# Kernel tuning notes

Hardware: AMD Instinct MI355X
Metric: run time of the kernel (lower is better)

Reference implementation:

```python
import jax, jax.numpy as jnp
import numpy as np

D_MODEL = 1024
N_HEADS = 16
D_KEYS = 64
GROUP_POSITIONS = [list(range(g * 32, (g + 1) * 32)) for g in range(4)]


def _make_tables(group_positions, dim):
    # InGroup table: pe[j,i] = (j/Lg) * L0 / 10000^(2*(i//2)/dim)
    L0 = len(group_positions[0])
    rows = []
    for grp in group_positions:
        Lg = len(grp)
        for j in range(Lg):
            rows.append([j / Lg * L0 / np.power(10000.0, 2 * (i // 2) / dim) for i in range(dim)])
    pe = np.array(rows)
    ingroup = np.concatenate([np.sin(pe[:, 0::2]), np.cos(pe[:, 1::2])], axis=1).astype(np.float32)
    # Sequence (group) table: pe[j,i] = grp[0] / 10000^(j/Lg), constant over i
    rows = []
    for grp in group_positions:
        Lg = len(grp)
        for j in range(Lg):
            rows.append([grp[0] / np.power(10000.0, j / Lg) for _ in range(dim)])
    pe = np.array(rows)
    seq = np.concatenate([np.sin(pe[:, 0::2]), np.cos(pe[:, 1::2])], axis=1).astype(np.float32)
    return jnp.asarray(ingroup), jnp.asarray(seq)


def setup_inputs() -> dict:
    key = jax.random.key(0)
    ks = jax.random.split(key, 12)
    B, L, S = 64, 128, 128
    dqk = D_KEYS * N_HEADS
    sc_in = 1.0 / np.sqrt(D_MODEL)
    sc_out = 1.0 / np.sqrt(dqk)
    inp = {
        "queries": jax.random.normal(ks[0], (B, L, D_MODEL), jnp.float32),
        "keys": jax.random.normal(ks[1], (B, S, D_MODEL), jnp.float32),
        "values": jax.random.normal(ks[2], (B, S, D_MODEL), jnp.float32),
        "attn_mask": jnp.zeros((B, 1, L, S), dtype=bool),
        "Wq": jax.random.normal(ks[3], (D_MODEL, dqk), jnp.float32) * sc_in,
        "bq": jnp.zeros((dqk,), jnp.float32),
        "Wk": jax.random.normal(ks[4], (D_MODEL, dqk), jnp.float32) * sc_in,
        "bk": jnp.zeros((dqk,), jnp.float32),
        "Wv": jax.random.normal(ks[5], (D_MODEL, dqk), jnp.float32) * sc_in,
        "bv": jnp.zeros((dqk,), jnp.float32),
        "Wo": jax.random.normal(ks[6], (dqk, D_MODEL), jnp.float32) * sc_out,
        "bo": jnp.zeros((D_MODEL,), jnp.float32),
    }
    pos_ingroup, pos_seq = _make_tables(GROUP_POSITIONS, D_KEYS)
    inp["pos_ingroup"] = pos_ingroup  # [n_pos, d_keys]
    inp["pos_seq"] = pos_seq          # [n_pos, d_keys]
    return inp


def _rope(x, pos):
    # x: [B, H, L, D]; pos: [L, D]
    sin, cos = jnp.split(pos, 2, axis=-1)
    sin_pos = jnp.stack([sin, sin], axis=-1).reshape(pos.shape)
    cos_pos = jnp.stack([cos, cos], axis=-1).reshape(pos.shape)
    rot = jnp.stack([-x[..., 1::2], x[..., ::2]], axis=-1).reshape(x.shape)
    return x * cos_pos + rot * sin_pos


def reference(queries, keys, values, attn_mask, Wq, bq, Wk, bk, Wv, bv, Wo, bo, pos_ingroup, pos_seq):
    B, L, _ = queries.shape
    S = keys.shape[1]
    H, E = N_HEADS, D_KEYS
    q = (queries @ Wq + bq).reshape(B, L, H, E).transpose(0, 2, 1, 3)  # [B,H,L,E]
    k = (keys @ Wk + bk).reshape(B, S, H, E).transpose(0, 2, 1, 3)
    v = (values @ Wv + bv).reshape(B, S, H, E).transpose(0, 2, 1, 3)
    # group-sequence in-group RoPE, then group RoPE (tables gathered at arange positions)
    q = _rope(_rope(q, pos_ingroup[:L]), pos_seq[:L])
    k = _rope(_rope(k, pos_ingroup[:S]), pos_seq[:S])
    # inner full attention on [B,L,H,E] layout
    scale = 1.0 / jnp.sqrt(jnp.asarray(E, q.dtype))
    scores = jnp.einsum("bhle,bhse->bhls", q, k) * scale
    scores = jnp.where(attn_mask, jnp.asarray(-jnp.inf, scores.dtype), scores)
    attn = jax.nn.softmax(scores, axis=-1)  # [B,H,L,S]
    out = jnp.einsum("bhls,bhsd->blhd", attn, v).reshape(B, L, H * E)
    return out @ Wo + bo, attn
```

## Files before the change

kernel.cpp:

```cpp
#include <hip/hip_runtime.h>
#include <cstdint>

typedef float f32x4 __attribute__((ext_vector_type(4)));
typedef __bf16 bf16x8 __attribute__((ext_vector_type(8)));

typedef __attribute__((address_space(3))) uint32_t lds_u32;
typedef __attribute__((address_space(1))) const uint32_t glb_u32;

#define GLOAD_LDS16(gp, lp) \
  __builtin_amdgcn_global_load_lds((glb_u32*)(uintptr_t)(gp), (lds_u32*)(uintptr_t)(lp), 16, 0, 0)

__device__ inline unsigned short f2bf(float f) {
  union { float f; uint32_t u; } v; v.f = f;
  uint32_t u = v.u;
  return (unsigned short)((u + 0x7fffu + ((u >> 16) & 1u)) >> 16);
}

__global__ void prep_w(const float* __restrict__ wq, const float* __restrict__ wk,
                       const float* __restrict__ wv, const float* __restrict__ wo,
                       unsigned short* __restrict__ wt)
{
  __shared__ float t[64][65];
  const int z = blockIdx.z;
  const float* W = (z == 0) ? wq : (z == 1) ? wk : (z == 2) ? wv : wo;
  unsigned short* Wt = wt + (size_t)z * 1048576;
  const int n0 = blockIdx.x * 64, k0 = blockIdx.y * 64;
  const int tx = threadIdx.x & 63, ty = threadIdx.x >> 6;
#pragma unroll
  for (int i = 0; i < 16; i++) {
    int row = i * 4 + ty;
    t[row][tx] = W[(size_t)(k0 + row) * 1024 + n0 + tx];
  }
  __syncthreads();
#pragma unroll
  for (int i = 0; i < 16; i++) {
    int row = i * 4 + ty;
    Wt[(size_t)(n0 + row) * 1024 + k0 + tx] = f2bf(t[tx][row]);
  }
}

__global__ void comb_kernel(const float* __restrict__ ing, const float* __restrict__ seq,
                            float* __restrict__ cosc, float* __restrict__ sinc)
{
  int idx = blockIdx.x * 256 + threadIdx.x;
  int j = idx >> 5, i = idx & 31;
  float s1 = ing[j * 64 + i], c1 = ing[j * 64 + 32 + i];
  float s2 = seq[j * 64 + i], c2 = seq[j * 64 + 32 + i];
  cosc[idx] = c1 * c2 - s1 * s2;
  sinc[idx] = s1 * c2 + c1 * s2;
}

__global__ void cvt_kernel(const float* __restrict__ q, const float* __restrict__ k,
                           const float* __restrict__ v, unsigned short* __restrict__ dst)
{
  const int z = blockIdx.z;
  const float* src = (z == 0) ? q : (z == 1) ? k : v;
  unsigned short* d = dst + (size_t)z * 8388608;
  size_t i = ((size_t)blockIdx.x * 256 + threadIdx.x) * 4;
  float4 f = *(const float4*)&src[i];
  ushort4 o;
  o.x = f2bf(f.x); o.y = f2bf(f.y); o.z = f2bf(f.z); o.w = f2bf(f.w);
  *(ushort4*)&d[i] = o;
}

__global__ __launch_bounds__(512, 2)
void gemm256(const unsigned short* __restrict__ Abase,
             const unsigned short* __restrict__ Bbase,
             const float* __restrict__ b0, const float* __restrict__ b1,
             const float* __restrict__ b2,
             unsigned short* __restrict__ qb, unsigned short* __restrict__ kb,
             unsigned short* __restrict__ vtb,
             const float* __restrict__ cosc, const float* __restrict__ sinc)
{
  __shared__ __attribute__((aligned(16))) unsigned short lds[2][2][16384];

  const int tid = threadIdx.x;
  const int lane = tid & 63;
  const int wave = tid >> 6;
  const int quad = lane >> 4;
  const int l15 = lane & 15;

  const int z = blockIdx.z;
  const int tileM = blockIdx.x * 256;
  const int tileN = blockIdx.y * 256;

  const unsigned short* A = Abase + (size_t)z * (8192u * 1024u);
  const unsigned short* B = Bbase + (size_t)z * (1024u * 1024u);

  const int wm = (wave >> 2) * 128;
  const int wn = (wave & 3) * 64;

  int oA[8], oB[4];
#pragma unroll
  for (int a = 0; a < 8; a++) oA[a] = (wm + a * 16 + l15) * 64;
#pragma unroll
  for (int n = 0; n < 4; n++) oB[n] = (wn + n * 16 + l15) * 64;
  const int cp0 = (quad ^ (l15 & 7)) * 8;
  const int cp1 = ((4 + quad) ^ (l15 & 7)) * 8;

  const unsigned short* sA[2][2];
  const unsigned short* sB[2][2];
#pragma unroll
  for (int h = 0; h < 2; h++)
#pragma unroll
    for (int j = 0; j < 2; j++) {
      int g = tid + j * 512;
      int lr = g >> 3;
      int gc = (g & 7) ^ (lr & 7);
      sA[h][j] = A + (size_t)(tileM + h * 128 + lr) * 1024 + gc * 8;
      sB[h][j] = B + (size_t)(tileN + h * 128 + lr) * 1024 + gc * 8;
    }

  auto stageA = [&](int buf, int kn) {
#pragma unroll
    for (int h = 0; h < 2; h++)
#pragma unroll
      for (int j = 0; j < 2; j++)
        GLOAD_LDS16(sA[h][j] + kn, &lds[buf][0][h * 8192 + (wave * 64 + j * 512) * 8]);
  };
  auto stageB = [&](int buf, int kn) {
#pragma unroll
    for (int h = 0; h < 2; h++)
#pragma unroll
      for (int j = 0; j < 2; j++)
        GLOAD_LDS16(sB[h][j] + kn, &lds[buf][1][h * 8192 + (wave * 64 + j * 512) * 8]);
  };

  f32x4 acc[8][4];
#pragma unroll
  for (int a = 0; a < 8; a++)
#pragma unroll
    for (int n = 0; n < 4; n++)
      acc[a][n] = (f32x4){0.f, 0.f, 0.f, 0.f};

  stageA(0, 0);
  stageB(0, 0);
  asm volatile("s_waitcnt vmcnt(0)" ::: "memory");
  __builtin_amdgcn_sched_barrier(0);
  __builtin_amdgcn_s_barrier();

  for (int t = 0; t < 16; ++t) {
    const int cur = t & 1;
    const int nxt = cur ^ 1;
    const unsigned short* As_ = &lds[cur][0][0];
    const unsigned short* Bs_ = &lds[cur][1][0];
    const int kn = (t + 1) * 64;
    bf16x8 af[4], bfr[4];

#pragma unroll
    for (int i = 0; i < 4; i++) af[i] = *(const bf16x8*)&As_[oA[i] + cp0];
#pragma unroll
    for (int n = 0; n < 4; n++) bfr[n] = *(const bf16x8*)&Bs_[oB[n] + cp0];
    if (t < 15) stageA(nxt, kn);
    __builtin_amdgcn_s_barrier();
    asm volatile("s_waitcnt lgkmcnt(0)" ::: "memory");
    __builtin_amdgcn_sched_barrier(0);
    __builtin_amdgcn_s_setprio(1);
#pragma unroll
    for (int i = 0; i < 4; i++)
#pragma unroll
      for (int n = 0; n < 4; n++)
        acc[i][n] = __builtin_amdgcn_mfma_f32_16x16x32_bf16(af[i], bfr[n], acc[i][n], 0, 0, 0);
    __builtin_amdgcn_s_setprio(0);
    __builtin_amdgcn_s_barrier();

#pragma unroll
    for (int i = 0; i < 4; i++) af[i] = *(const bf16x8*)&As_[oA[4 + i] + cp0];
    if (t < 15) stageB(nxt, kn);
    __builtin_amdgcn_s_barrier();
    asm volatile("s_waitcnt lgkmcnt(0)" ::: "memory");
    __builtin_amdgcn_sched_barrier(0);
    __builtin_amdgcn_s_setprio(1);
#pragma unroll
    for (int i = 0; i < 4; i++)
#pragma unroll
      for (int n = 0; n < 4; n++)
        acc[4 + i][n] = __builtin_amdgcn_mfma_f32_16x16x32_bf16(af[i], bfr[n], acc[4 + i][n], 0, 0, 0);
    __builtin_amdgcn_s_setprio(0);
    __builtin_amdgcn_s_barrier();

#pragma unroll
    for (int i = 0; i < 4; i++) af[i] = *(const bf16x8*)&As_[oA[i] + cp1];
#pragma unroll
    for (int n = 0; n < 4; n++) bfr[n] = *(const bf16x8*)&Bs_[oB[n] + cp1];
    __builtin_amdgcn_s_barrier();
    asm volatile("s_waitcnt lgkmcnt(0)" ::: "memory");
    __builtin_amdgcn_sched_barrier(0);
    __builtin_amdgcn_s_setprio(1);
#pragma unroll
    for (int i = 0; i < 4; i++)
#pragma unroll
      for (int n = 0; n < 4; n++)
        acc[i][n] = __builtin_amdgcn_mfma_f32_16x16x32_bf16(af[i], bfr[n], acc[i][n], 0, 0, 0);
    __builtin_amdgcn_s_setprio(0);
    __builtin_amdgcn_s_barrier();

#pragma unroll
    for (int i = 0; i < 4; i++) af[i] = *(const bf16x8*)&As_[oA[4 + i] + cp1];
    __builtin_amdgcn_s_barrier();
    asm volatile("s_waitcnt lgkmcnt(0)" ::: "memory");
    __builtin_amdgcn_sched_barrier(0);
    __builtin_amdgcn_s_setprio(1);
#pragma unroll
    for (int i = 0; i < 4; i++)
#pragma unroll
      for (int n = 0; n < 4; n++)
        acc[4 + i][n] = __builtin_amdgcn_mfma_f32_16x16x32_bf16(af[i], bfr[n], acc[4 + i][n], 0, 0, 0);
    __builtin_amdgcn_s_setprio(0);
    asm volatile("s_waitcnt vmcnt(0)" ::: "memory");
    __builtin_amdgcn_sched_barrier(0);
    __builtin_amdgcn_s_barrier();
  }

  const float* bias = (z == 0) ? b0 : (z == 1) ? b1 : b2;
  unsigned short* outq = (z == 0) ? qb : kb;
#pragma unroll
  for (int n = 0; n < 4; n++) {
    int cg = tileN + wn + n * 16 + l15;
    float bv_ = bias[cg];
    int h = cg >> 6, e = cg & 63;
#pragma unroll
    for (int a = 0; a < 8; a++)
#pragma unroll
      for (int reg = 0; reg < 4; reg++) {
        int r = tileM + wm + a * 16 + quad * 4 + reg;
        int bb = r >> 7, l = r & 127;
        float v = acc[a][n][reg] + bv_;
        if (z == 2) {
          vtb[(((size_t)bb * 16 + h) * 64 + e) * 128 + l] = f2bf(v);
        } else {
          float other = __shfl_xor(v, 1);
          float cs = cosc[l * 32 + (e >> 1)];
          float sn = sinc[l * 32 + (e >> 1)];
          float res = v * cs + ((e & 1) ? other : -other) * sn;
          outq[(((size_t)bb * 16 + h) * 128 + l) * 64 + e] = f2bf(res);
        }
      }
  }
}

__global__ __launch_bounds__(256, 2)
void gemm_bt(const unsigned short* __restrict__ Abase,
             const unsigned short* __restrict__ Bbase,
             const float* __restrict__ b0, const float* __restrict__ b1,
             const float* __restrict__ b2,
             unsigned short* __restrict__ qb, unsigned short* __restrict__ kb,
             unsigned short* __restrict__ vtb,
             float* __restrict__ outf,
             const float* __restrict__ cosc, const float* __restrict__ sinc,
             int final_mode)
{
  __shared__ __attribute__((aligned(16))) unsigned short As[128 * 64];
  __shared__ __attribute__((aligned(16))) unsigned short Bs[128 * 64];

  const int tid = threadIdx.x;
  const int lane = tid & 63;
  const int wave = tid >> 6;
  const int quad = lane >> 4;
  const int l15 = lane & 15;

  const int z = blockIdx.z;
  const int tileM = blockIdx.x * 128;
  const int tileN = blockIdx.y * 128;
  const int K = 1024;

  const unsigned short* A = Abase + (size_t)z * (8192u * 1024u);
  const unsigned short* B = Bbase + (size_t)z * (1024u * 1024u);

  const int wm = (wave >> 1) * 64;
  const int wn = (wave & 1) * 64;

  f32x4 acc[4][4];
#pragma unroll
  for (int a = 0; a < 4; a++)
#pragma unroll
    for (int n = 0; n < 4; n++)
      acc[a][n] = (f32x4){0.f, 0.f, 0.f, 0.f};

  for (int k0 = 0; k0 < K; k0 += 64) {
#pragma unroll
    for (int cc = 0; cc < 4; cc++) {
      int c = wave * 4 + cc;
      int s = c * 64 + lane;
      int row = s >> 3;
      int gc = (s & 7) ^ (row & 7);
      const unsigned short* ga = A + (size_t)(tileM + row) * K + k0 + gc * 8;
      const unsigned short* gb = B + (size_t)(tileN + row) * K + k0 + gc * 8;
      GLOAD_LDS16(ga, &As[c * 512]);
      GLOAD_LDS16(gb, &Bs[c * 512]);
    }
    __syncthreads();

#pragma unroll
    for (int ks = 0; ks < 2; ks++) {
      bf16x8 af[4], bfr[4];
#pragma unroll
      for (int a = 0; a < 4; a++) {
        int r = wm + a * 16 + l15;
        int cp = (ks * 4 + quad) ^ (r & 7);
        af[a] = *(const bf16x8*)&As[(r * 8 + cp) * 8];
      }
#pragma unroll
      for (int n = 0; n < 4; n++) {
        int r = wn + n * 16 + l15;
        int cp = (ks * 4 + quad) ^ (r & 7);
        bfr[n] = *(const bf16x8*)&Bs[(r * 8 + cp) * 8];
      }
#pragma unroll
      for (int a = 0; a < 4; a++)
#pragma unroll
        for (int n = 0; n < 4; n++)
          acc[a][n] = __builtin_amdgcn_mfma_f32_16x16x32_bf16(af[a], bfr[n], acc[a][n], 0, 0, 0);
    }
    __syncthreads();
  }

  if (final_mode) {
#pragma unroll
    for (int n = 0; n < 4; n++) {
      int cg = tileN + wn + n * 16 + l15;
      float bias = b0[cg];
#pragma unroll
      for (int a = 0; a < 4; a++)
#pragma unroll
        for (int reg = 0; reg < 4; reg++) {
          int r = tileM + wm + a * 16 + quad * 4 + reg;
          outf[(size_t)r * 1024 + cg] = acc[a][n][reg] + bias;
        }
    }
  } else {
    const float* bias = (z == 0) ? b0 : (z == 1) ? b1 : b2;
    unsigned short* outq = (z == 0) ? qb : kb;
#pragma unroll
    for (int n = 0; n < 4; n++) {
      int cg = tileN + wn + n * 16 + l15;
      float bv_ = bias[cg];
      int h = cg >> 6, e = cg & 63;
#pragma unroll
      for (int a = 0; a < 4; a++)
#pragma unroll
        for (int reg = 0; reg < 4; reg++) {
          int r = tileM + wm + a * 16 + quad * 4 + reg;
          int bb = r >> 7, l = r & 127;
          float v = acc[a][n][reg] + bv_;
          if (z == 2) {
            vtb[(((size_t)bb * 16 + h) * 64 + e) * 128 + l] = f2bf(v);
          } else {
            float other = __shfl_xor(v, 1);
            float cs = cosc[l * 32 + (e >> 1)];
            float sn = sinc[l * 32 + (e >> 1)];
            float res = v * cs + ((e & 1) ? other : -other) * sn;
            outq[(((size_t)bb * 16 + h) * 128 + l) * 64 + e] = f2bf(res);
          }
        }
    }
  }
}

__global__ __launch_bounds__(256, 2)
void attn_kernel(const unsigned short* __restrict__ qb,
                 const unsigned short* __restrict__ kb,
                 const unsigned short* __restrict__ vtb,
                 const unsigned char* __restrict__ mask,
                 float* __restrict__ attn_out,
                 unsigned short* __restrict__ ob)
{
  __shared__ __attribute__((aligned(16))) unsigned short Pb[128 * 136];
  const int tid = threadIdx.x;
  const int lane = tid & 63;
  const int wave = tid >> 6;
  const int quad = lane >> 4;
  const int l15 = lane & 15;
  const int bh = blockIdx.x;
  const int b = bh >> 4;
  const int h = bh & 15;

  const unsigned short* q = qb + (size_t)bh * 128 * 64;
  const unsigned short* k = kb + (size_t)bh * 128 * 64;
  const unsigned short* vt = vtb + (size_t)bh * 64 * 128;

  f32x4 sacc[2][8];
#pragma unroll
  for (int mt = 0; mt < 2; mt++)
#pragma unroll
    for (int nt = 0; nt < 8; nt++)
      sacc[mt][nt] = (f32x4){0.f, 0.f, 0.f, 0.f};

#pragma unroll
  for (int ks = 0; ks < 2; ks++) {
    bf16x8 aq[2], bk[8];
#pragma unroll
    for (int mt = 0; mt < 2; mt++)
      aq[mt] = *(const bf16x8*)&q[(size_t)(wave * 32 + mt * 16 + l15) * 64 + ks * 32 + quad * 8];
#pragma unroll
    for (int nt = 0; nt < 8; nt++)
      bk[nt] = *(const bf16x8*)&k[(size_t)(nt * 16 + l15) * 64 + ks * 32 + quad * 8];
#pragma unroll
    for (int mt = 0; mt < 2; mt++)
#pragma unroll
      for (int nt = 0; nt < 8; nt++)
        sacc[mt][nt] = __builtin_amdgcn_mfma_f32_16x16x32_bf16(aq[mt], bk[nt], sacc[mt][nt], 0, 0, 0);
  }

  const float scale = 0.125f;
#pragma unroll
  for (int mt = 0; mt < 2; mt++) {
#pragma unroll
    for (int reg = 0; reg < 4; reg++) {
      int r = wave * 32 + mt * 16 + quad * 4 + reg;
      const unsigned char* mrow = mask + ((size_t)b * 128 + r) * 128;
      float sv[8];
#pragma unroll
      for (int nt = 0; nt < 8; nt++) {
        float x = sacc[mt][nt][reg] * scale;
        if (mrow[nt * 16 + l15]) x = -__builtin_inff();
        sv[nt] = x;
      }
      float m = sv[0];
#pragma unroll
      for (int nt = 1; nt < 8; nt++) m = fmaxf(m, sv[nt]);
#pragma unroll
      for (int off = 1; off < 16; off <<= 1) m = fmaxf(m, __shfl_xor(m, off));
      float s = 0.f;
#pragma unroll
      for (int nt = 0; nt < 8; nt++) { sv[nt] = __expf(sv[nt] - m); s += sv[nt]; }
#pragma unroll
      for (int off = 1; off < 16; off <<= 1) s += __shfl_xor(s, off);
      float inv = 1.0f / s;
      float* arow = attn_out + ((size_t)bh * 128 + r) * 128;
#pragma unroll
      for (int nt = 0; nt < 8; nt++) {
        float p = sv[nt] * inv;
        arow[nt * 16 + l15] = p;
        Pb[r * 136 + nt * 16 + l15] = f2bf(p);
      }
    }
  }
  __syncthreads();

  f32x4 oacc[2][4];
#pragma unroll
  for (int mt = 0; mt < 2; mt++)
#pragma unroll
    for (int nt = 0; nt < 4; nt++)
      oacc[mt][nt] = (f32x4){0.f, 0.f, 0.f, 0.f};

#pragma unroll
  for (int ks = 0; ks < 4; ks++) {
    bf16x8 bv[4], ap[2];
#pragma unroll
    for (int nt = 0; nt < 4; nt++)
      bv[nt] = *(const bf16x8*)&vt[(size_t)(nt * 16 + l15) * 128 + ks * 32 + quad * 8];
#pragma unroll
    for (int mt = 0; mt < 2; mt++)
      ap[mt] = *(const bf16x8*)&Pb[(size_t)(wave * 32 + mt * 16 + l15) * 136 + ks * 32 + quad * 8];
#pragma unroll
    for (int mt = 0; mt < 2; mt++)
#pragma unroll
      for (int nt = 0; nt < 4; nt++)
        oacc[mt][nt] = __builtin_amdgcn_mfma_f32_16x16x32_bf16(ap[mt], bv[nt], oacc[mt][nt], 0, 0, 0);
  }

#pragma unroll
  for (int mt = 0; mt < 2; mt++)
#pragma unroll
    for (int nt = 0; nt < 4; nt++)
#pragma unroll
      for (int reg = 0; reg < 4; reg++) {
        int r = wave * 32 + mt * 16 + quad * 4 + reg;
        int e = nt * 16 + l15;
        ob[((size_t)b * 128 + r) * 1024 + h * 64 + e] = f2bf(oacc[mt][nt][reg]);
      }
}

extern "C" void kernel_launch(void* const* d_in, const int* in_sizes, int n_in,
                              void* d_out, int out_size, void* d_ws, size_t ws_size,
                              hipStream_t stream)
{
  const float* queries = (const float*)d_in[0];
  const float* keys    = (const float*)d_in[1];
  const float* values  = (const float*)d_in[2];
  const unsigned char* mask = (const unsigned char*)d_in[3];
  const float* Wq = (const float*)d_in[4];
  const float* bq = (const float*)d_in[5];
  const float* Wk = (const float*)d_in[6];
  const float* bk = (const float*)d_in[7];
  const float* Wv = (const float*)d_in[8];
  const float* bv = (const float*)d_in[9];
  const float* Wo = (const float*)d_in[10];
  const float* bo = (const float*)d_in[11];
  const float* ping = (const float*)d_in[12];
  const float* pseq = (const float*)d_in[13];

  float* out  = (float*)d_out;
  float* attn = out + 8388608;
  unsigned short* Xbf = (unsigned short*)attn;

  char* ws = (char*)d_ws;
  unsigned short* Wt  = (unsigned short*)(ws);
  float* cosc = (float*)(ws + 8388608);
  float* sinc = (float*)(ws + 8388608 + 16384);
  unsigned short* qbuf = (unsigned short*)(ws + 8421376);
  unsigned short* kbuf = (unsigned short*)(ws + 8421376 + 16777216);
  unsigned short* vtbuf= (unsigned short*)(ws + 8421376 + 2*16777216);
  unsigned short* obuf = (unsigned short*)(ws + 8421376 + 3*16777216);

  prep_w<<<dim3(16, 16, 4), 256, 0, stream>>>(Wq, Wk, Wv, Wo, Wt);
  comb_kernel<<<16, 256, 0, stream>>>(ping, pseq, cosc, sinc);
  cvt_kernel<<<dim3(8192, 1, 3), 256, 0, stream>>>(queries, keys, values, Xbf);
  gemm256<<<dim3(32, 4, 3), 512, 0, stream>>>(Xbf, Wt, bq, bk, bv,
                                              qbuf, kbuf, vtbuf, cosc, sinc);
  attn_kernel<<<dim3(1024), 256, 0, stream>>>(qbuf, kbuf, vtbuf, mask, attn, obuf);
  gemm_bt<<<dim3(64, 8, 1), 256, 0, stream>>>(obuf, Wt + 3 * 1048576, bo, bo, bo,
                                              qbuf, kbuf, vtbuf, out,
                                              cosc, sinc, 1);
}
```

Measured before the change: 391.8 us.

## Shrink QKV GEMM tile to 128x256 with triple-buffered LDS pipeline

Result: faster. 347.3 us (-11.3%).

```diff
diff --git a/kernel.cpp b/kernel.cpp
--- a/kernel.cpp
+++ b/kernel.cpp
@@ -64,15 +64,15 @@
 }
 
 __global__ __launch_bounds__(512, 2)
-void gemm256(const unsigned short* __restrict__ Abase,
-             const unsigned short* __restrict__ Bbase,
-             const float* __restrict__ b0, const float* __restrict__ b1,
-             const float* __restrict__ b2,
-             unsigned short* __restrict__ qb, unsigned short* __restrict__ kb,
-             unsigned short* __restrict__ vtb,
-             const float* __restrict__ cosc, const float* __restrict__ sinc)
-{
-  __shared__ __attribute__((aligned(16))) unsigned short lds[2][2][16384];
+void gemm_qkv(const unsigned short* __restrict__ Abase,
+              const unsigned short* __restrict__ Bbase,
+              const float* __restrict__ b0, const float* __restrict__ b1,
+              const float* __restrict__ b2,
+              unsigned short* __restrict__ qb, unsigned short* __restrict__ kb,
+              unsigned short* __restrict__ vtb,
+              const float* __restrict__ cosc, const float* __restrict__ sinc)
+{
+  __shared__ __attribute__((aligned(16))) unsigned short lds[3][24576];
 
   const int tid = threadIdx.x;
   const int lane = tid & 63;
@@ -81,78 +81,80 @@
   const int l15 = lane & 15;
 
   const int z = blockIdx.z;
-  const int tileM = blockIdx.x * 256;
+  const int tileM = blockIdx.x * 128;
   const int tileN = blockIdx.y * 256;
 
   const unsigned short* A = Abase + (size_t)z * (8192u * 1024u);
   const unsigned short* B = Bbase + (size_t)z * (1024u * 1024u);
 
-  const int wm = (wave >> 2) * 128;
+  const int wm = (wave >> 2) * 64;
   const int wn = (wave & 3) * 64;
 
-  int oA[8], oB[4];
-#pragma unroll
-  for (int a = 0; a < 8; a++) oA[a] = (wm + a * 16 + l15) * 64;
-#pragma unroll
-  for (int n = 0; n < 4; n++) oB[n] = (wn + n * 16 + l15) * 64;
+  int oA[4], oB[4];
+#pragma unroll
+  for (int a = 0; a < 4; a++) oA[a] = (wm + a * 16 + l15) * 64;
+#pragma unroll
+  for (int n = 0; n < 4; n++) oB[n] = 8192 + (wn + n * 16 + l15) * 64;
   const int cp0 = (quad ^ (l15 & 7)) * 8;
   const int cp1 = ((4 + quad) ^ (l15 & 7)) * 8;
 
-  const unsigned short* sA[2][2];
-  const unsigned short* sB[2][2];
-#pragma unroll
-  for (int h = 0; h < 2; h++)
-#pragma unroll
-    for (int j = 0; j < 2; j++) {
-      int g = tid + j * 512;
-      int lr = g >> 3;
-      int gc = (g & 7) ^ (lr & 7);
-      sA[h][j] = A + (size_t)(tileM + h * 128 + lr) * 1024 + gc * 8;
-      sB[h][j] = B + (size_t)(tileN + h * 128 + lr) * 1024 + gc * 8;
-    }
-
-  auto stageA = [&](int buf, int kn) {
-#pragma unroll
-    for (int h = 0; h < 2; h++)
-#pragma unroll
-      for (int j = 0; j < 2; j++)
-        GLOAD_LDS16(sA[h][j] + kn, &lds[buf][0][h * 8192 + (wave * 64 + j * 512) * 8]);
+  const unsigned short* sA[2];
+  const unsigned short* sB[4];
+#pragma unroll
+  for (int j = 0; j < 2; j++) {
+    int g = tid + j * 512;
+    int lr = g >> 3;
+    int gc = (g & 7) ^ (lr & 7);
+    sA[j] = A + (size_t)(tileM + lr) * 1024 + gc * 8;
+  }
+#pragma unroll
+  for (int j = 0; j < 4; j++) {
+    int g = tid + j * 512;
+    int lr = g >> 3;
+    int gc = (g & 7) ^ (lr & 7);
+    sB[j] = B + (size_t)(tileN + lr) * 1024 + gc * 8;
+  }
+
+  auto stage = [&](int s) {
+    const int bidx = s % 3;
+    const int ko = s * 64;
+#pragma unroll
+    for (int j = 0; j < 2; j++)
+      GLOAD_LDS16(sA[j] + ko, &lds[bidx][(wave * 64 + j * 512) * 8]);
+#pragma unroll
+    for (int j = 0; j < 4; j++)
+      GLOAD_LDS16(sB[j] + ko, &lds[bidx][8192 + (wave * 64 + j * 512) * 8]);
   };
-  auto stageB = [&](int buf, int kn) {
-#pragma unroll
-    for (int h = 0; h < 2; h++)
-#pragma unroll
-      for (int j = 0; j < 2; j++)
-        GLOAD_LDS16(sB[h][j] + kn, &lds[buf][1][h * 8192 + (wave * 64 + j * 512) * 8]);
-  };
-
-  f32x4 acc[8][4];
-#pragma unroll
-  for (int a = 0; a < 8; a++)
+
+  f32x4 acc[4][4];
+#pragma unroll
+  for (int a = 0; a < 4; a++)
 #pragma unroll
     for (int n = 0; n < 4; n++)
       acc[a][n] = (f32x4){0.f, 0.f, 0.f, 0.f};
 
-  stageA(0, 0);
-  stageB(0, 0);
-  asm volatile("s_waitcnt vmcnt(0)" ::: "memory");
-  __builtin_amdgcn_sched_barrier(0);
-  __builtin_amdgcn_s_barrier();
+  stage(0);
+  stage(1);
 
   for (int t = 0; t < 16; ++t) {
-    const int cur = t & 1;
-    const int nxt = cur ^ 1;
-    const unsigned short* As_ = &lds[cur][0][0];
-    const unsigned short* Bs_ = &lds[cur][1][0];
-    const int kn = (t + 1) * 64;
-    bf16x8 af[4], bfr[4];
-
-#pragma unroll
-    for (int i = 0; i < 4; i++) af[i] = *(const bf16x8*)&As_[oA[i] + cp0];
-#pragma unroll
-    for (int n = 0; n < 4; n++) bfr[n] = *(const bf16x8*)&Bs_[oB[n] + cp0];
-    if (t < 15) stageA(nxt, kn);
+    if (t < 15) { asm volatile("s_waitcnt vmcnt(6)" ::: "memory"); }
+    else        { asm volatile("s_waitcnt vmcnt(0)" ::: "memory"); }
+    __builtin_amdgcn_sched_barrier(0);
     __builtin_amdgcn_s_barrier();
+
+    const unsigned short* L = &lds[t % 3][0];
+    bf16x8 a0[4], a1[4], f0[4], f1[4];
+#pragma unroll
+    for (int i = 0; i < 4; i++) a0[i] = *(const bf16x8*)&L[oA[i] + cp0];
+#pragma unroll
+    for (int i = 0; i < 4; i++) a1[i] = *(const bf16x8*)&L[oA[i] + cp1];
+#pragma unroll
+    for (int n = 0; n < 4; n++) f0[n] = *(const bf16x8*)&L[oB[n] + cp0];
+#pragma unroll
+    for (int n = 0; n < 4; n++) f1[n] = *(const bf16x8*)&L[oB[n] + cp1];
+
+    if (t < 14) stage(t + 2);
+
     asm volatile("s_waitcnt lgkmcnt(0)" ::: "memory");
     __builtin_amdgcn_sched_barrier(0);
     __builtin_amdgcn_s_setprio(1);
@@ -160,56 +162,13 @@
     for (int i = 0; i < 4; i++)
 #pragma unroll
       for (int n = 0; n < 4; n++)
-        acc[i][n] = __builtin_amdgcn_mfma_f32_16x16x32_bf16(af[i], bfr[n], acc[i][n], 0, 0, 0);
+        acc[i][n] = __builtin_amdgcn_mfma_f32_16x16x32_bf16(a0[i], f0[n], acc[i][n], 0, 0, 0);
+#pragma unroll
+    for (int i = 0; i < 4; i++)
+#pragma unroll
+      for (int n = 0; n < 4; n++)
+        acc[i][n] = __builtin_amdgcn_mfma_f32_16x16x32_bf16(a1[i], f1[n], acc[i][n], 0, 0, 0);
     __builtin_amdgcn_s_setprio(0);
-    __builtin_amdgcn_s_barrier();
-
-#pragma unroll
-    for (int i = 0; i < 4; i++) af[i] = *(const bf16x8*)&As_[oA[4 + i] + cp0];
-    if (t < 15) stageB(nxt, kn);
-    __builtin_amdgcn_s_barrier();
-    asm volatile("s_waitcnt lgkmcnt(0)" ::: "memory");
-    __builtin_amdgcn_sched_barrier(0);
-    __builtin_amdgcn_s_setprio(1);
-#pragma unroll
-    for (int i = 0; i < 4; i++)
-#pragma unroll
-      for (int n = 0; n < 4; n++)
-        acc[4 + i][n] = __builtin_amdgcn_mfma_f32_16x16x32_bf16(af[i], bfr[n], acc[4 + i][n], 0, 0, 0);
-    __builtin_amdgcn_s_setprio(0);
-    __builtin_amdgcn_s_barrier();
-
-#pragma unroll
-    for (int i = 0; i < 4; i++) af[i] = *(const bf16x8*)&As_[oA[i] + cp1];
-#pragma unroll
-    for (int n = 0; n < 4; n++) bfr[n] = *(const bf16x8*)&Bs_[oB[n] + cp1];
-    __builtin_amdgcn_s_barrier();
-    asm volatile("s_waitcnt lgkmcnt(0)" ::: "memory");
-    __builtin_amdgcn_sched_barrier(0);
-    __builtin_amdgcn_s_setprio(1);
-#pragma unroll
-    for (int i = 0; i < 4; i++)
-#pragma unroll
-      for (int n = 0; n < 4; n++)
-        acc[i][n] = __builtin_amdgcn_mfma_f32_16x16x32_bf16(af[i], bfr[n], acc[i][n], 0, 0, 0);
-    __builtin_amdgcn_s_setprio(0);
-    __builtin_amdgcn_s_barrier();
-
-#pragma unroll
-    for (int i = 0; i < 4; i++) af[i] = *(const bf16x8*)&As_[oA[4 + i] + cp1];
-    __builtin_amdgcn_s_barrier();
-    asm volatile("s_waitcnt lgkmcnt(0)" ::: "memory");
-    __builtin_amdgcn_sched_barrier(0);
-    __builtin_amdgcn_s_setprio(1);
-#pragma unroll
-    for (int i = 0; i < 4; i++)
-#pragma unroll
-      for (int n = 0; n < 4; n++)
-        acc[4 + i][n] = __builtin_amdgcn_mfma_f32_16x16x32_bf16(af[i], bfr[n], acc[4 + i][n], 0, 0, 0);
-    __builtin_amdgcn_s_setprio(0);
-    asm volatile("s_waitcnt vmcnt(0)" ::: "memory");
-    __builtin_amdgcn_sched_barrier(0);
-    __builtin_amdgcn_s_barrier();
   }
 
   const float* bias = (z == 0) ? b0 : (z == 1) ? b1 : b2;
@@ -220,7 +179,7 @@
     float bv_ = bias[cg];
     int h = cg >> 6, e = cg & 63;
 #pragma unroll
-    for (int a = 0; a < 8; a++)
+    for (int a = 0; a < 4; a++)
 #pragma unroll
       for (int reg = 0; reg < 4; reg++) {
         int r = tileM + wm + a * 16 + quad * 4 + reg;
@@ -508,8 +467,8 @@
   prep_w<<<dim3(16, 16, 4), 256, 0, stream>>>(Wq, Wk, Wv, Wo, Wt);
   comb_kernel<<<16, 256, 0, stream>>>(ping, pseq, cosc, sinc);
   cvt_kernel<<<dim3(8192, 1, 3), 256, 0, stream>>>(queries, keys, values, Xbf);
-  gemm256<<<dim3(32, 4, 3), 512, 0, stream>>>(Xbf, Wt, bq, bk, bv,
-                                              qbuf, kbuf, vtbuf, cosc, sinc);
+  gemm_qkv<<<dim3(64, 4, 3), 512, 0, stream>>>(Xbf, Wt, bq, bk, bv,
+                                               qbuf, kbuf, vtbuf, cosc, sinc);
   attn_kernel<<<dim3(1024), 256, 0, stream>>>(qbuf, kbuf, vtbuf, mask, attn, obuf);
   gemm_bt<<<dim3(64, 8, 1), 256, 0, stream>>>(obuf, Wt + 3 * 1048576, bo, bo, bo,
                                               qbuf, kbuf, vtbuf, out,
```
